# Optimization experiments

Measured on AMD Instinct MI355X. Metric: run time of the kernel, lower is better.

The kernel has to match this reference:

```python
import jax, jax.numpy as jnp
import numpy as np

F_N = 100000   # binary factors
V_N = 30000    # variables
E_N = 1000000  # GAT edges
DEG = 3        # sources per v2f target
D = 15         # msg_dim / domain size
HID = 60       # in_channels - prefix_dim
IN = 64        # in_channels
OUT = 32       # out_channels
T_N = 2 * F_N          # number of v2f (= f2v) messages
N_N = V_N + 5 * F_N    # GAT nodes


def _gru(x, h, w_ih, w_hh, b_ih, b_hh):
    gi = x @ w_ih.T + b_ih
    gh = h @ w_hh.T + b_hh
    ir, iz, i_n = jnp.split(gi, 3, axis=1)
    hr, hz, h_n = jnp.split(gh, 3, axis=1)
    r = jax.nn.sigmoid(ir + hr)
    z = jax.nn.sigmoid(iz + hz)
    n = jnp.tanh(i_n + r * h_n)
    return (1.0 - z) * n + z * h


def _gat(x, src, dst, W, a_src, a_dst, bias, heads, out_dim, concat):
    n = x.shape[0]
    h = (x @ W).reshape(n, heads, out_dim)
    e = jax.nn.leaky_relu((h * a_src).sum(-1)[src] + (h * a_dst).sum(-1)[dst], 0.2)
    emax = jax.ops.segment_max(e, dst, num_segments=n)
    w = jnp.exp(e - emax[dst])
    den = jax.ops.segment_sum(w, dst, num_segments=n)
    alpha = w / (den[dst] + 1e-16)
    out = jax.ops.segment_sum(h[src] * alpha[:, :, None], dst, num_segments=n)
    out = out.reshape(n, heads * out_dim) if concat else out.mean(axis=1)
    return out + bias


def _attn(q, k, Wq, Wk, Ws, b):
    return jax.nn.sigmoid(jnp.concatenate([q @ Wq.T, k @ Wk.T], axis=1) @ Ws.T + b)


def _forward(msgs, cost_tensors, func_embed, v2f_hidden, f2v_hidden, embed_table,
             w_ih1, w_hh1, b_ih1, b_hh1, w_ih2, w_hh2, b_ih2, b_hh2,
             W1, as1, ad1, bb1, W2, as2, ad2, bb2, W3, as3, ad3, bb3,
             W4, as4, ad4, bb4, Wq, Wk, Ws, bs_att,
             edge_index, var_colors,
             msg_rv2f_idxes, msg_cv2f_idxes, msg_f2rv_idxes, msg_f2cv_idxes,
             msg_src_idxes, msg_trg_idxes, msg_f2v_per_v_idxes,
             embed_trg_idxes, embed_src_idxes, v2f_scatter_idxes,
             f2v_per_v_scatter_idxes, f_batch, rv_idxes, cv_idxes):
    Fn = cost_tensors.shape[0]
    T = msg_trg_idxes.shape[0]
    # ---- min-plus BP factor updates ----
    m_rv2f = msgs[msg_rv2f_idxes]
    m_cv2f = msgs[msg_cv2f_idxes]
    m_f2rv = jnp.min(cost_tensors + m_cv2f[:, None, :], axis=2)
    m_f2cv = jnp.min(cost_tensors + m_rv2f[:, :, None], axis=1)
    msgs = msgs.at[msg_f2rv_idxes].set(m_f2rv).at[msg_f2cv_idxes].set(m_f2cv)
    # ---- GRU state updates (inputs detached as in source) ----
    v2f_h = _gru(jax.lax.stop_gradient(jnp.concatenate([m_rv2f, m_cv2f], axis=0)),
                 v2f_hidden, w_ih1, w_hh1, b_ih1, b_hh1)
    f2v_h = _gru(jax.lax.stop_gradient(jnp.concatenate([m_f2rv, m_f2cv], axis=0)),
                 f2v_hidden, w_ih2, w_hh2, b_ih2, b_hh2)
    # ---- node features with 4-dim one-hot type prefixes (VAR_ID/V2F_ID/F2V_ID) ----
    ve = embed_table[var_colors]
    def pref(t, v):
        p = jnp.zeros((v.shape[0], 4), v.dtype).at[:, t].set(1.0)
        return jnp.concatenate([p, v], axis=1)
    x = jnp.concatenate([pref(0, ve), func_embed, pref(1, v2f_h), pref(2, f2v_h)], axis=0)
    # ---- GAT stack with self loops ----
    n = x.shape[0]
    loops = jnp.arange(n, dtype=edge_index.dtype)
    src = jnp.concatenate([edge_index[0], loops])
    dst = jnp.concatenate([edge_index[1], loops])
    x = jax.nn.leaky_relu(_gat(x, src, dst, W1, as1, ad1, bb1, 4, 8, True), 0.01)
    x = jax.nn.leaky_relu(_gat(x, src, dst, W2, as2, ad2, bb2, 4, 8, True), 0.01)
    x = jax.nn.leaky_relu(_gat(x, src, dst, W3, as3, ad3, bb3, 4, 8, True), 0.01)
    x = jax.nn.leaky_relu(_gat(x, src, dst, W4, as4, ad4, bb4, 4, OUT, False), 0.01)
    # ---- scatter-softmax attention aggregation over v2f targets ----
    msg_src = msgs[msg_src_idxes]
    msg_trg = msgs[msg_trg_idxes]
    e_src = x[embed_src_idxes]
    e_trg = x[embed_trg_idxes]
    e_trg_rep = e_trg[v2f_scatter_idxes]  # == repeat_interleave by degree (idxes sorted)
    deg = jax.ops.segment_sum(jnp.ones((v2f_scatter_idxes.shape[0],), x.dtype),
                              v2f_scatter_idxes, num_segments=T)
    scores = _attn(e_trg_rep, e_src, Wq, Wk, Ws, bs_att)   # [TD, 1]
    trg_scores = _attn(e_trg, e_trg, Wq, Wk, Ws, bs_att)   # [T, 1]
    smax = jax.ops.segment_max(scores, v2f_scatter_idxes, num_segments=T)
    w = jnp.exp(scores - smax[v2f_scatter_idxes])
    den = jax.ops.segment_sum(w, v2f_scatter_idxes, num_segments=T)
    aw = w / den[v2f_scatter_idxes]
    weighted = jax.ops.segment_sum(msg_src[:, :, None] * aw[:, None, :],
                                   v2f_scatter_idxes, num_segments=T)  # [T, D, 1]
    weighted = weighted.mean(axis=-1) * deg[:, None]
    mean_scores = jax.ops.segment_sum(scores, v2f_scatter_idxes, num_segments=T) / deg[:, None]
    damped = jax.nn.softmax(jnp.stack([mean_scores, trg_scores], axis=1), axis=1)  # [T, 2, 1]
    v2f = weighted[:, :, None] * damped[:, 0][:, None, :] + msg_trg[:, :, None] * damped[:, 1][:, None, :]
    v2f = v2f.mean(axis=-1)
    v2f = v2f - v2f.min(axis=1, keepdims=True)
    msgs = msgs.at[msg_trg_idxes].set(v2f)
    # ---- beliefs, entropy, loss ----
    belief = jax.ops.segment_sum(msgs[msg_f2v_per_v_idxes], f2v_per_v_scatter_idxes,
                                 num_segments=V_N)
    dist = jax.nn.softmax(-belief, axis=1)
    ent = -(dist * jnp.log2(dist + 1e-6)).sum(axis=1).mean()
    drv = dist[rv_idxes]
    dcv = dist[cv_idxes]
    per_f = jnp.einsum('fi,fij,fj->f', drv, cost_tensors, dcv)
    loss = jax.ops.segment_sum(per_f, f_batch, num_segments=1).mean() + 0.1 * ent
    vr = jnp.argmax(drv, axis=1)
    vc = jnp.argmax(dcv, axis=1)
    cost = cost_tensors[jnp.arange(Fn), vr, vc]
    cost_mean = jax.ops.segment_sum(cost, f_batch, num_segments=1).mean()
    return loss, cost_mean


def setup_inputs():
    key = jax.random.key(0)
    ks = jax.random.split(key, 24)
    f32 = jnp.float32
    s = 0.1
    inp = {}
    inp['msgs'] = jax.random.normal(ks[0], (4 * F_N, D), f32)
    inp['cost_tensors'] = jax.random.uniform(ks[1], (F_N, D, D), f32)
    inp['func_embed'] = jax.random.normal(ks[2], (F_N, IN), f32) * s
    inp['v2f_hidden'] = jax.random.normal(ks[3], (T_N, HID), f32) * s
    inp['f2v_hidden'] = jax.random.normal(ks[4], (T_N, HID), f32) * s
    inp['embed_table'] = jax.random.normal(ks[5], (100, HID), f32) * s
    inp['w_ih1'] = jax.random.normal(ks[6], (3 * HID, D), f32) * s
    inp['w_hh1'] = jax.random.normal(ks[7], (3 * HID, HID), f32) * s
    inp['b_ih1'] = jnp.zeros((3 * HID,), f32)
    inp['b_hh1'] = jnp.zeros((3 * HID,), f32)
    inp['w_ih2'] = jax.random.normal(ks[8], (3 * HID, D), f32) * s
    inp['w_hh2'] = jax.random.normal(ks[9], (3 * HID, HID), f32) * s
    inp['b_ih2'] = jnp.zeros((3 * HID,), f32)
    inp['b_hh2'] = jnp.zeros((3 * HID,), f32)
    inp['W1'] = jax.random.normal(ks[10], (IN, 32), f32) * s
    inp['as1'] = jax.random.normal(ks[11], (4, 8), f32) * s
    inp['ad1'] = jax.random.normal(ks[12], (4, 8), f32) * s
    inp['bb1'] = jnp.zeros((32,), f32)
    inp['W2'] = jax.random.normal(ks[13], (32, 32), f32) * s
    inp['as2'] = jax.random.normal(ks[14], (4, 8), f32) * s
    inp['ad2'] = jax.random.normal(ks[15], (4, 8), f32) * s
    inp['bb2'] = jnp.zeros((32,), f32)
    inp['W3'] = jax.random.normal(ks[16], (32, 32), f32) * s
    inp['as3'] = jax.random.normal(ks[17], (4, 8), f32) * s
    inp['ad3'] = jax.random.normal(ks[18], (4, 8), f32) * s
    inp['bb3'] = jnp.zeros((32,), f32)
    inp['W4'] = jax.random.normal(ks[19], (32, 4 * OUT), f32) * s
    inp['as4'] = jax.random.normal(ks[20], (4, OUT), f32) * s
    inp['ad4'] = jax.random.normal(ks[21], (4, OUT), f32) * s
    inp['bb4'] = jnp.zeros((OUT,), f32)
    inp['Wq'] = jax.random.normal(ks[22], (OUT, OUT), f32) * s
    inp['Wk'] = jax.random.normal(ks[23], (OUT, OUT), f32) * s
    k2 = jax.random.split(jax.random.fold_in(key, 1), 8)
    inp['Ws'] = jax.random.normal(k2[0], (1, 2 * OUT), f32) * s
    inp['bs_att'] = jnp.zeros((1,), f32)
    inp['edge_index'] = jax.random.randint(k2[1], (2, E_N), 0, N_N, jnp.int32)
    inp['var_colors'] = jax.random.randint(k2[2], (V_N,), 0, 100, jnp.int32)
    inp['msg_rv2f_idxes'] = jnp.arange(0, F_N, dtype=jnp.int32)
    inp['msg_cv2f_idxes'] = jnp.arange(F_N, 2 * F_N, dtype=jnp.int32)
    inp['msg_f2rv_idxes'] = jnp.arange(2 * F_N, 3 * F_N, dtype=jnp.int32)
    inp['msg_f2cv_idxes'] = jnp.arange(3 * F_N, 4 * F_N, dtype=jnp.int32)
    inp['msg_src_idxes'] = jax.random.randint(k2[3], (T_N * DEG,), 2 * F_N, 4 * F_N, jnp.int32)
    inp['msg_trg_idxes'] = jnp.arange(0, T_N, dtype=jnp.int32)
    inp['msg_f2v_per_v_idxes'] = jnp.arange(2 * F_N, 4 * F_N, dtype=jnp.int32)
    inp['embed_trg_idxes'] = V_N + F_N + inp['msg_trg_idxes']
    inp['embed_src_idxes'] = V_N + F_N + inp['msg_src_idxes']
    inp['v2f_scatter_idxes'] = jnp.repeat(jnp.arange(T_N, dtype=jnp.int32), DEG)
    inp['f2v_per_v_scatter_idxes'] = jnp.concatenate([
        jnp.arange(V_N, dtype=jnp.int32),
        jax.random.randint(k2[4], (T_N - V_N,), 0, V_N, jnp.int32)])
    inp['f_batch'] = jnp.zeros((F_N,), jnp.int32)
    inp['rv_idxes'] = jax.random.randint(k2[5], (F_N,), 0, V_N, jnp.int32)
    inp['cv_idxes'] = jax.random.randint(k2[6], (F_N,), 0, V_N, jnp.int32)
    return inp


def reference(msgs, cost_tensors, func_embed, v2f_hidden, f2v_hidden, embed_table,
              w_ih1, w_hh1, b_ih1, b_hh1, w_ih2, w_hh2, b_ih2, b_hh2,
              W1, as1, ad1, bb1, W2, as2, ad2, bb2, W3, as3, ad3, bb3,
              W4, as4, ad4, bb4, Wq, Wk, Ws, bs_att,
              edge_index, var_colors,
              msg_rv2f_idxes, msg_cv2f_idxes, msg_f2rv_idxes, msg_f2cv_idxes,
              msg_src_idxes, msg_trg_idxes, msg_f2v_per_v_idxes,
              embed_trg_idxes, embed_src_idxes, v2f_scatter_idxes,
              f2v_per_v_scatter_idxes, f_batch, rv_idxes, cv_idxes):
    return _forward(msgs, cost_tensors, func_embed, v2f_hidden, f2v_hidden, embed_table,
                    w_ih1, w_hh1, b_ih1, b_hh1, w_ih2, w_hh2, b_ih2, b_hh2,
                    W1, as1, ad1, bb1, W2, as2, ad2, bb2, W3, as3, ad3, bb3,
                    W4, as4, ad4, bb4, Wq, Wk, Ws, bs_att,
                    edge_index, var_colors,
                    msg_rv2f_idxes, msg_cv2f_idxes, msg_f2rv_idxes, msg_f2cv_idxes,
                    msg_src_idxes, msg_trg_idxes, msg_f2v_per_v_idxes,
                    embed_trg_idxes, embed_src_idxes, v2f_scatter_idxes,
                    f2v_per_v_scatter_idxes, f_batch, rv_idxes, cv_idxes)
```

## Files before the change

kernel.cpp:

```cpp
#include <hip/hip_runtime.h>

#define F_N 100000
#define V_N 30000
#define DD 15
#define TILE 225
#define NSLOT 256
#define MPB 8

static const int BELIEF_OFF = 0;
static const int SLOTP_OFF  = 450048;
static const int SLOTC_OFF  = 450304;
static const int ENT_OFF    = 450560;
static const int DIST_OFF   = 450576;
static const int AMAX_OFF   = 900576;
static const int ZERO_N     = 450576;

__global__ void k_init(float* __restrict__ ws) {
    int i = blockIdx.x * blockDim.x + threadIdx.x;
    if (i < ZERO_N) ws[i] = 0.0f;
}

__global__ __launch_bounds__(256) void k_minplus_scatter(
        const float* __restrict__ msgs,
        const float* __restrict__ cost,
        const int*   __restrict__ scat,
        float* __restrict__ belief) {
    __shared__ float tile[MPB * TILE];
    __shared__ float mlds[2 * MPB * DD];
    int f0  = blockIdx.x * MPB;
    int tid = threadIdx.x;

    const float* src = cost + (size_t)f0 * TILE;
    for (int e = tid; e < MPB * TILE; e += 256) tile[e] = src[e];
    if (tid < 2 * MPB * DD) {
        mlds[tid] = (tid < MPB * DD) ? msgs[(size_t)f0 * DD + tid]
                                     : msgs[(size_t)(F_N + f0) * DD + (tid - MPB * DD)];
    }
    __syncthreads();

    int q = tid >> 5;
    int r = tid & 31;
    if (r < 30) {
        bool is_row = (r < DD);
        int i = is_row ? r : (r - DD);
        int f = f0 + q;
        const float* mb = is_row ? &mlds[MPB * DD + q * DD] : &mlds[q * DD];
        const float* Cf = &tile[q * TILE];
        float mn = 1e30f;
#pragma unroll
        for (int k = 0; k < DD; ++k) {
            int a = is_row ? (i * DD + k) : (k * DD + i);
            mn = fminf(mn, Cf[a] + mb[k]);
        }
        int v = scat[is_row ? f : (F_N + f)];
        atomicAdd(&belief[v * DD + i], mn);
    }
}

__global__ void k_softmax_ent(const float* __restrict__ belief,
                              float* __restrict__ dist,
                              int*   __restrict__ amax,
                              float* __restrict__ ent) {
    int v = blockIdx.x * blockDim.x + threadIdx.x;
    float entp = 0.0f;
    if (v < V_N) {
        float b[DD];
        float mn = 1e30f;
#pragma unroll
        for (int k = 0; k < DD; ++k) { b[k] = belief[v * DD + k]; mn = fminf(mn, b[k]); }
        float e[DD];
        float den = 0.0f;
#pragma unroll
        for (int k = 0; k < DD; ++k) { e[k] = expf(mn - b[k]); den += e[k]; }
        float inv = 1.0f / den;
        float best = -1.0f;
        int am = 0;
#pragma unroll
        for (int k = 0; k < DD; ++k) {
            float dk = e[k] * inv;
            dist[v * DD + k] = dk;
            entp -= dk * log2f(dk + 1e-6f);
            if (dk > best) { best = dk; am = k; }
        }
        amax[v] = am;
    }
#pragma unroll
    for (int off = 32; off > 0; off >>= 1) entp += __shfl_down(entp, off, 64);
    if ((threadIdx.x & 63) == 0) atomicAdd(ent, entp);
}

__global__ __launch_bounds__(256) void k_factor_loss(
        const float* __restrict__ cost,
        const float* __restrict__ dist,
        const int*   __restrict__ amax,
        const int*   __restrict__ rv_idx,
        const int*   __restrict__ cv_idx,
        float* __restrict__ slotP,
        float* __restrict__ slotC) {
    int gtid = blockIdx.x * 256 + threadIdx.x;
    int f    = gtid >> 6;
    int lane = threadIdx.x & 63;
    float s = 0.0f, c = 0.0f;
    if (f < F_N) {
        int rv = rv_idx[f], cv = cv_idx[f];
        const float* dr = dist + (size_t)rv * DD;
        const float* dc = dist + (size_t)cv * DD;
        const float* Cf = cost + (size_t)f * TILE;
#pragma unroll
        for (int t = 0; t < 4; ++t) {
            int e = lane + t * 64;
            if (e < TILE) {
                int i = e / DD;
                int j = e - i * DD;
                s += dr[i] * Cf[e] * dc[j];
            }
        }
        if (lane == 0) c = Cf[amax[rv] * DD + amax[cv]];
    }
#pragma unroll
    for (int off = 32; off > 0; off >>= 1) s += __shfl_down(s, off, 64);
    __shared__ float sP[4], sC[4];
    int w = threadIdx.x >> 6;
    if (lane == 0) { sP[w] = s; sC[w] = c; }
    __syncthreads();
    if (threadIdx.x == 0) {
        float tp = sP[0] + sP[1] + sP[2] + sP[3];
        float tc = sC[0] + sC[1] + sC[2] + sC[3];
        int slot = blockIdx.x & (NSLOT - 1);
        atomicAdd(&slotP[slot], tp);
        atomicAdd(&slotC[slot], tc);
    }
}

__global__ void k_final(const float* __restrict__ slotP,
                        const float* __restrict__ slotC,
                        const float* __restrict__ ent,
                        float* __restrict__ out) {
    int t = threadIdx.x;
    float p = slotP[t], c = slotC[t];
#pragma unroll
    for (int off = 32; off > 0; off >>= 1) {
        p += __shfl_down(p, off, 64);
        c += __shfl_down(c, off, 64);
    }
    __shared__ float sp[4], sc[4];
    if ((t & 63) == 0) { sp[t >> 6] = p; sc[t >> 6] = c; }
    __syncthreads();
    if (t == 0) {
        float tp = sp[0] + sp[1] + sp[2] + sp[3];
        float tc = sc[0] + sc[1] + sc[2] + sc[3];
        out[0] = tp + 0.1f * (ent[0] / (float)V_N);
        out[1] = tc;
    }
}

extern "C" void kernel_launch(void* const* d_in, const int* in_sizes, int n_in,
                              void* d_out, int out_size, void* d_ws, size_t ws_size,
                              hipStream_t stream) {
    const float* msgs = (const float*)d_in[0];
    const float* cost = (const float*)d_in[1];
    const int* scat   = (const int*)d_in[46];
    const int* rv     = (const int*)d_in[48];
    const int* cv     = (const int*)d_in[49];

    float* ws     = (float*)d_ws;
    float* belief = ws + BELIEF_OFF;
    float* slotP  = ws + SLOTP_OFF;
    float* slotC  = ws + SLOTC_OFF;
    float* ent    = ws + ENT_OFF;
    float* dist   = ws + DIST_OFF;
    int*   amax   = (int*)(ws + AMAX_OFF);
    float* out    = (float*)d_out;

    k_init<<<(ZERO_N + 255) / 256, 256, 0, stream>>>(ws);
    k_minplus_scatter<<<F_N / MPB, 256, 0, stream>>>(msgs, cost, scat, belief);
    k_softmax_ent<<<(V_N + 255) / 256, 256, 0, stream>>>(belief, dist, amax, ent);
    k_factor_loss<<<(F_N * 64 + 255) / 256, 256, 0, stream>>>(cost, dist, amax, rv, cv, slotP, slotC);
    k_final<<<1, 256, 0, stream>>>(slotP, slotC, ent, out);
}
```

Measured before the change: 93.10 us.

## Replace atomic belief scatter with per-variable linked-list gather of messages

The min-plus kernel now writes each factor-to-variable message to a dense buffer instead of atomically adding it into the variable beliefs. A new kernel builds per-variable linked lists with atomicExch on a head array. The softmax kernel then walks each variable's list and sums the messages in registers. The aim is to remove about three million float atomics and the zeroing of the belief buffer. In exchange it adds an extra kernel, writes and re-reads a large message buffer, and leaves each of only 30k threads chasing dependent pointers serially. The cost tile load is also vectorised to float4.

```diff
diff --git a/kernel.cpp b/kernel.cpp
--- a/kernel.cpp
+++ b/kernel.cpp
@@ -4,34 +4,40 @@
 #define V_N 30000
 #define DD 15
 #define TILE 225
+#define T_N (2 * F_N)
 #define NSLOT 256
 #define MPB 8
 
-static const int BELIEF_OFF = 0;
-static const int SLOTP_OFF  = 450048;
-static const int SLOTC_OFF  = 450304;
-static const int ENT_OFF    = 450560;
-static const int DIST_OFF   = 450576;
-static const int AMAX_OFF   = 900576;
-static const int ZERO_N     = 450576;
-
-__global__ void k_init(float* __restrict__ ws) {
+static const size_t M_OFF     = 0;
+static const size_t DIST_OFF  = 3000000;
+static const size_t HEAD_OFF  = 3450048;
+static const size_t NEXT_OFF  = 3480064;
+static const size_t AMAX_OFF  = 3680064;
+static const size_t SLOTP_OFF = 3710080;
+static const size_t SLOTC_OFF = 3710336;
+static const size_t ENT_OFF   = 3710592;
+
+__global__ void k_init(int* __restrict__ head, float* __restrict__ slots) {
     int i = blockIdx.x * blockDim.x + threadIdx.x;
-    if (i < ZERO_N) ws[i] = 0.0f;
-}
-
-__global__ __launch_bounds__(256) void k_minplus_scatter(
+    if (i < V_N) head[i] = -1;
+    if (i < 2 * NSLOT + 1) slots[i] = 0.0f;
+}
+
+__global__ __launch_bounds__(256) void k_minplus(
         const float* __restrict__ msgs,
         const float* __restrict__ cost,
-        const int*   __restrict__ scat,
-        float* __restrict__ belief) {
-    __shared__ float tile[MPB * TILE];
+        float* __restrict__ m) {
+    __shared__ __align__(16) float tile[MPB * TILE];
     __shared__ float mlds[2 * MPB * DD];
     int f0  = blockIdx.x * MPB;
     int tid = threadIdx.x;
 
-    const float* src = cost + (size_t)f0 * TILE;
-    for (int e = tid; e < MPB * TILE; e += 256) tile[e] = src[e];
+    const float4* src4 = reinterpret_cast<const float4*>(cost + (size_t)f0 * TILE);
+    float4* dst4 = reinterpret_cast<float4*>(tile);
+    if (tid < 225) {
+        dst4[tid] = src4[tid];
+        dst4[tid + 225] = src4[tid + 225];
+    }
     if (tid < 2 * MPB * DD) {
         mlds[tid] = (tid < MPB * DD) ? msgs[(size_t)f0 * DD + tid]
                                      : msgs[(size_t)(F_N + f0) * DD + (tid - MPB * DD)];
@@ -52,22 +58,42 @@
             int a = is_row ? (i * DD + k) : (k * DD + i);
             mn = fminf(mn, Cf[a] + mb[k]);
         }
-        int v = scat[is_row ? f : (F_N + f)];
-        atomicAdd(&belief[v * DD + i], mn);
-    }
-}
-
-__global__ void k_softmax_ent(const float* __restrict__ belief,
-                              float* __restrict__ dist,
-                              int*   __restrict__ amax,
-                              float* __restrict__ ent) {
+        size_t t = is_row ? (size_t)f : (size_t)(F_N + f);
+        m[t * DD + i] = mn;
+    }
+}
+
+__global__ void k_build(const int* __restrict__ scat,
+                        int* __restrict__ head,
+                        int* __restrict__ next) {
+    int t = blockIdx.x * blockDim.x + threadIdx.x;
+    if (t < T_N) {
+        int v = scat[t];
+        int old = atomicExch(&head[v], t);
+        next[t] = old;
+    }
+}
+
+__global__ void k_gather_softmax(const float* __restrict__ m,
+                                 const int* __restrict__ head,
+                                 const int* __restrict__ next,
+                                 float* __restrict__ dist,
+                                 int*   __restrict__ amax,
+                                 float* __restrict__ ent) {
     int v = blockIdx.x * blockDim.x + threadIdx.x;
     float entp = 0.0f;
     if (v < V_N) {
         float b[DD];
+#pragma unroll
+        for (int k = 0; k < DD; ++k) b[k] = 0.0f;
+        for (int t = head[v]; t >= 0; t = next[t]) {
+            const float* mr = m + (size_t)t * DD;
+#pragma unroll
+            for (int k = 0; k < DD; ++k) b[k] += mr[k];
+        }
         float mn = 1e30f;
 #pragma unroll
-        for (int k = 0; k < DD; ++k) { b[k] = belief[v * DD + k]; mn = fminf(mn, b[k]); }
+        for (int k = 0; k < DD; ++k) mn = fminf(mn, b[k]);
         float e[DD];
         float den = 0.0f;
 #pragma unroll
@@ -147,10 +173,8 @@
     if ((t & 63) == 0) { sp[t >> 6] = p; sc[t >> 6] = c; }
     __syncthreads();
     if (t == 0) {
-        float tp = sp[0] + sp[1] + sp[2] + sp[3];
-        float tc = sc[0] + sc[1] + sc[2] + sc[3];
-        out[0] = tp + 0.1f * (ent[0] / (float)V_N);
-        out[1] = tc;
+        out[0] = (sp[0] + sp[1] + sp[2] + sp[3]) + 0.1f * (ent[0] / (float)V_N);
+        out[1] = (sc[0] + sc[1] + sc[2] + sc[3]);
     }
 }
 
@@ -163,18 +187,21 @@
     const int* rv     = (const int*)d_in[48];
     const int* cv     = (const int*)d_in[49];
 
-    float* ws     = (float*)d_ws;
-    float* belief = ws + BELIEF_OFF;
-    float* slotP  = ws + SLOTP_OFF;
-    float* slotC  = ws + SLOTC_OFF;
-    float* ent    = ws + ENT_OFF;
-    float* dist   = ws + DIST_OFF;
-    int*   amax   = (int*)(ws + AMAX_OFF);
-    float* out    = (float*)d_out;
-
-    k_init<<<(ZERO_N + 255) / 256, 256, 0, stream>>>(ws);
-    k_minplus_scatter<<<F_N / MPB, 256, 0, stream>>>(msgs, cost, scat, belief);
-    k_softmax_ent<<<(V_N + 255) / 256, 256, 0, stream>>>(belief, dist, amax, ent);
+    float* ws    = (float*)d_ws;
+    float* m     = ws + M_OFF;
+    float* dist  = ws + DIST_OFF;
+    int*   head  = (int*)(ws + HEAD_OFF);
+    int*   next  = (int*)(ws + NEXT_OFF);
+    int*   amax  = (int*)(ws + AMAX_OFF);
+    float* slotP = ws + SLOTP_OFF;
+    float* slotC = ws + SLOTC_OFF;
+    float* ent   = ws + ENT_OFF;
+    float* out   = (float*)d_out;
+
+    k_init<<<(V_N + 255) / 256, 256, 0, stream>>>(head, slotP);
+    k_minplus<<<F_N / MPB, 256, 0, stream>>>(msgs, cost, m);
+    k_build<<<(T_N + 255) / 256, 256, 0, stream>>>(scat, head, next);
+    k_gather_softmax<<<(V_N + 255) / 256, 256, 0, stream>>>(m, head, next, dist, amax, ent);
     k_factor_loss<<<(F_N * 64 + 255) / 256, 256, 0, stream>>>(cost, dist, amax, rv, cv, slotP, slotC);
     k_final<<<1, 256, 0, stream>>>(slotP, slotC, ent, out);
 }
```

Result: slower. 99.04 us (+6.4%).
